# Kernel optimization log

Hardware: AMD Instinct MI355X
Metric: run time of the kernel (lower is better)

## Reference

```python
import jax, jax.numpy as jnp
import numpy as np

N_NODES = 50000
N_EDGES = 800000


def setup_inputs() -> dict:
    key = jax.random.key(0)
    k1, k2, k3, k4 = jax.random.split(key, 4)
    x = jax.random.normal(k1, (N_NODES, 100), dtype=jnp.float32)
    edge_index = jax.random.randint(k2, (2, N_EDGES), 0, N_NODES, dtype=jnp.int64)
    W1 = jax.random.normal(k3, (100, 128), dtype=jnp.float32) * 0.1
    b1 = jnp.zeros((128,), dtype=jnp.float32)
    W2 = jax.random.normal(k4, (128, 64), dtype=jnp.float32) * 0.1
    b2 = jnp.zeros((64,), dtype=jnp.float32)
    return {"x": x, "edge_index": edge_index, "W1": W1, "b1": b1, "W2": W2, "b2": b2}


def _gcn_norm(edge_index, n_nodes):
    # PyG GCNConv default: add self-loops, then symmetric normalization
    row, col = edge_index[0], edge_index[1]
    loop = jnp.arange(n_nodes, dtype=row.dtype)
    row = jnp.concatenate([row, loop])
    col = jnp.concatenate([col, loop])
    deg = jax.ops.segment_sum(jnp.ones_like(col, dtype=jnp.float32), col,
                              num_segments=n_nodes)
    dinv = jnp.where(deg > 0, jax.lax.rsqrt(deg), 0.0)
    norm = dinv[row] * dinv[col]  # [E + N]
    return row, col, norm


def _gcn_conv(x, W, b, row, col, norm, n_nodes):
    h = x @ W                       # [N, out] linear transform first (PyG order)
    msg = norm[:, None] * h[row]    # gather + scale over edges
    agg = jax.ops.segment_sum(msg, col, num_segments=n_nodes)  # scatter-add
    return agg + b


def reference(x, edge_index, W1, b1, W2, b2):
    n = x.shape[0]
    row, col, norm = _gcn_norm(edge_index, n)
    h = _gcn_conv(x, W1, b1, row, col, norm, n)
    h = jax.nn.relu(h)
    out = _gcn_conv(h, W2, b2, row, col, norm, n)
    return out
```

## Files before the change

kernel.cpp:

```cpp
#include <hip/hip_runtime.h>
#include <hip/hip_fp16.h>

#define DIV_UP(a,b) (((a)+(b)-1)/(b))

typedef _Float16 half8 __attribute__((ext_vector_type(8)));
typedef float f32x4 __attribute__((ext_vector_type(4)));

#define BUK_BITS 8
#define BUK_SIZE 256
#define BUK_CAP  6144
#define CSR_CAP  8192
#define MAXBUK   256
#define NBLK_BUCKET 256
#define CHUNK_MAX 3136

#define SWZ(row, colh) ((colh) ^ (((row) & 7) << 3))


__device__ __forceinline__ int edge_at(const void* ei, int mode64, int idx) {
  if (mode64) return (int)((const long long*)ei)[idx];
  return ((const int*)ei)[idx];
}

__global__ __launch_bounds__(256) void k_init(int* __restrict__ bcur,
                                              const float* __restrict__ W1,
                                              const float* __restrict__ W2,
                                              _Float16* __restrict__ Wt1,
                                              _Float16* __restrict__ Wt2) {
  int i = blockIdx.x * 256 + threadIdx.x;
  if (i < MAXBUK) bcur[i] = 0;
  if (i < 128 * 128) {
    int nc = i >> 7, k = i & 127;
    Wt1[i] = (k < 100) ? (_Float16)W1[k * 128 + nc] : (_Float16)0.f;
  } else if (i < 128 * 128 + 64 * 128) {
    int j = i - 128 * 128;
    int nc = j >> 7, k = j & 127;
    Wt2[j] = (_Float16)W2[k * 64 + nc];
  }
}

__global__ __launch_bounds__(256) void k_bucket(const void* __restrict__ ei,
                                                int* __restrict__ bcur,
                                                unsigned int* __restrict__ recs,
                                                int E, int nbuk) {
  __shared__ unsigned int lrec[CHUNK_MAX];
  __shared__ unsigned int sorted[CHUNK_MAX];
  __shared__ int hist[MAXBUK], lofs[MAXBUK], gbase[MAXBUK], cur[MAXBUK];
  __shared__ int smode;

  if (threadIdx.x < 64) {
    int v = ((const int*)ei)[2 * threadIdx.x + 1];
    unsigned long long b = __ballot(v == 0);
    if (threadIdx.x == 0) smode = (b == ~0ull) ? 1 : 0;
  }
  for (int i = threadIdx.x; i < nbuk; i += 256) hist[i] = 0;
  __syncthreads();
  const int m = smode;

  const int chunk = DIV_UP(E, gridDim.x);
  const int e0 = blockIdx.x * chunk;
  const int cnt = min(E, e0 + chunk) - e0;
  if (cnt <= 0) return;

  for (int i = threadIdx.x; i < cnt; i += 256) {
    int r = edge_at(ei, m, e0 + i);
    int c = edge_at(ei, m, E + e0 + i);
    unsigned int rec = ((unsigned)c << 16) | (unsigned)r;
    lrec[i] = rec;
    atomicAdd(&hist[c >> BUK_BITS], 1);
  }
  __syncthreads();

  if (threadIdx.x == 0) {
    int run = 0;
    for (int b = 0; b < nbuk; ++b) { lofs[b] = run; run += hist[b]; }
  }
  __syncthreads();
  for (int b = threadIdx.x; b < nbuk; b += 256) {
    gbase[b] = b * BUK_CAP + atomicAdd(&bcur[b], hist[b]);
    cur[b] = lofs[b];
  }
  __syncthreads();

  for (int i = threadIdx.x; i < cnt; i += 256) {
    unsigned int rec = lrec[i];
    int b = rec >> (16 + BUK_BITS);
    int p = atomicAdd(&cur[b], 1);
    sorted[p] = rec;
  }
  __syncthreads();

  for (int i = threadIdx.x; i < cnt; i += 256) {
    unsigned int rec = sorted[i];
    int b = rec >> (16 + BUK_BITS);
    recs[gbase[b] + i - lofs[b]] = rec;
  }
}

__global__ __launch_bounds__(256) void k_bdeg_fill(const int* __restrict__ bcur,
                                                   const unsigned int* __restrict__ recs,
                                                   float* __restrict__ dinv,
                                                   int2* __restrict__ rowinfo,
                                                   unsigned short* __restrict__ csr,
                                                   int n) {
  __shared__ int h[BUK_SIZE];
  __shared__ int psum[BUK_SIZE];
  __shared__ int curs[BUK_SIZE];
  __shared__ unsigned short lcsr[CSR_CAP];

  const int b = blockIdx.x, tid = threadIdx.x;
  const int base = b * BUK_CAP;
  const int cnt = bcur[b];
  const int n0 = b << BUK_BITS;
  const int nn = min(BUK_SIZE, n - n0);

  h[tid] = 0;
  __syncthreads();
  for (int i = tid; i < cnt; i += 256)
    atomicAdd(&h[(int)(recs[base + i] >> 16) - n0], 1);
  __syncthreads();

  const int deg = h[tid];
  const int plen = (deg + 7) & ~7;
  psum[tid] = plen;
  __syncthreads();
#pragma unroll
  for (int off2 = 1; off2 < 256; off2 <<= 1) {
    int v = (tid >= off2) ? psum[tid - off2] : 0;
    __syncthreads();
    psum[tid] += v;
    __syncthreads();
  }
  const int excl = psum[tid] - plen;
  const int ptot = psum[255];

  if (tid < nn) {
    rowinfo[n0 + tid] = make_int2(b * CSR_CAP + excl, plen);
    dinv[n0 + tid] = rsqrtf((float)deg + 1.0f);
    curs[tid] = excl;
  }
  for (int i = tid; i < ptot; i += 256) lcsr[i] = (unsigned short)n;
  __syncthreads();

  for (int i = tid; i < cnt; i += 256) {
    unsigned int rec = recs[base + i];
    int cl = (int)(rec >> 16) - n0;
    int p = atomicAdd(&curs[cl], 1);
    lcsr[p] = (unsigned short)(rec & 0xFFFFu);
  }
  __syncthreads();
  for (int i = tid; i < ptot; i += 256) csr[b * CSR_CAP + i] = lcsr[i];
}

__global__ __launch_bounds__(256) void k_convx(const float4* __restrict__ x4,
                                               const float* __restrict__ dinv,
                                               uint2* __restrict__ xh4,
                                               uint2* __restrict__ thh2,
                                               int n, int total) {
  int i = blockIdx.x * 256 + threadIdx.x;
  if (i < total) {
    int node = i >> 5;
    int lane = i & 31;
    uint2 val = make_uint2(0u, 0u);
    if (node < n && lane < 25) {
      float d = dinv[node];
      float4 v = x4[node * 25 + lane];
      union { uint2 u; __half2 hh[2]; } p;
      p.hh[0] = __halves2half2(__float2half_rn(d * v.x), __float2half_rn(d * v.y));
      p.hh[1] = __halves2half2(__float2half_rn(d * v.z), __float2half_rn(d * v.w));
      val = p.u;
    }
    xh4[i] = val;
  } else {
    int s = i - total;
    if (s < 16) thh2[(n << 4) + s] = make_uint2(0u, 0u);
  }
}

__device__ __forceinline__ float4 h4_to_f4(uint2 u) {
  union { uint2 u; __half2 h[2]; } p; p.u = u;
  float2 a = __half22float2(p.h[0]);
  float2 b = __half22float2(p.h[1]);
  return make_float4(a.x, a.y, b.x, b.y);
}
__device__ __forceinline__ void acc_add(float4& acc, float4 a) {
  acc.x += a.x; acc.y += a.y; acc.z += a.z; acc.w += a.w;
}

__global__ __launch_bounds__(256) void k_pull1(const int2* __restrict__ rowinfo,
                                               const unsigned short* __restrict__ csr,
                                               const uint2* __restrict__ xh4,
                                               const float* __restrict__ dinv,
                                               uint2* __restrict__ aggh4, int n) {
  int g = threadIdx.x / 25;
  int lane = threadIdx.x - g * 25;
  if (g >= 10) return;
  int node = blockIdx.x * 10 + g;
  if (node >= n) return;

  float4 acc = h4_to_f4(xh4[(node << 5) + lane]);
  int2 ri = rowinfo[node];
  int beg = ri.x, end = ri.x + ri.y;
  int j = beg;
  for (; j + 16 <= end; j += 16) {
    uint4 cw0 = *(const uint4*)&csr[j];
    uint4 cw1 = *(const uint4*)&csr[j + 8];
    int r0 = cw0.x & 0xFFFF, r1 = cw0.x >> 16;
    int r2 = cw0.y & 0xFFFF, r3 = cw0.y >> 16;
    int r4 = cw0.z & 0xFFFF, r5 = cw0.z >> 16;
    int r6 = cw0.w & 0xFFFF, r7 = cw0.w >> 16;
    int r8 = cw1.x & 0xFFFF, r9 = cw1.x >> 16;
    int rA = cw1.y & 0xFFFF, rB = cw1.y >> 16;
    int rC = cw1.z & 0xFFFF, rD = cw1.z >> 16;
    int rE = cw1.w & 0xFFFF, rF = cw1.w >> 16;
    float4 t0 = h4_to_f4(xh4[(r0 << 5) + lane]);
    float4 t1 = h4_to_f4(xh4[(r1 << 5) + lane]);
    float4 t2 = h4_to_f4(xh4[(r2 << 5) + lane]);
    float4 t3 = h4_to_f4(xh4[(r3 << 5) + lane]);
    float4 t4 = h4_to_f4(xh4[(r4 << 5) + lane]);
    float4 t5 = h4_to_f4(xh4[(r5 << 5) + lane]);
    float4 t6 = h4_to_f4(xh4[(r6 << 5) + lane]);
    float4 t7 = h4_to_f4(xh4[(r7 << 5) + lane]);
    float4 t8 = h4_to_f4(xh4[(r8 << 5) + lane]);
    float4 t9 = h4_to_f4(xh4[(r9 << 5) + lane]);
    float4 tA = h4_to_f4(xh4[(rA << 5) + lane]);
    float4 tB = h4_to_f4(xh4[(rB << 5) + lane]);
    float4 tC = h4_to_f4(xh4[(rC << 5) + lane]);
    float4 tD = h4_to_f4(xh4[(rD << 5) + lane]);
    float4 tE = h4_to_f4(xh4[(rE << 5) + lane]);
    float4 tF = h4_to_f4(xh4[(rF << 5) + lane]);
    acc_add(acc, t0); acc_add(acc, t1); acc_add(acc, t2); acc_add(acc, t3);
    acc_add(acc, t4); acc_add(acc, t5); acc_add(acc, t6); acc_add(acc, t7);
    acc_add(acc, t8); acc_add(acc, t9); acc_add(acc, tA); acc_add(acc, tB);
    acc_add(acc, tC); acc_add(acc, tD); acc_add(acc, tE); acc_add(acc, tF);
  }
  if (j < end) {
    uint4 cw = *(const uint4*)&csr[j];
    int r0 = cw.x & 0xFFFF, r1 = cw.x >> 16;
    int r2 = cw.y & 0xFFFF, r3 = cw.y >> 16;
    int r4 = cw.z & 0xFFFF, r5 = cw.z >> 16;
    int r6 = cw.w & 0xFFFF, r7 = cw.w >> 16;
    float4 t0 = h4_to_f4(xh4[(r0 << 5) + lane]);
    float4 t1 = h4_to_f4(xh4[(r1 << 5) + lane]);
    float4 t2 = h4_to_f4(xh4[(r2 << 5) + lane]);
    float4 t3 = h4_to_f4(xh4[(r3 << 5) + lane]);
    float4 t4 = h4_to_f4(xh4[(r4 << 5) + lane]);
    float4 t5 = h4_to_f4(xh4[(r5 << 5) + lane]);
    float4 t6 = h4_to_f4(xh4[(r6 << 5) + lane]);
    float4 t7 = h4_to_f4(xh4[(r7 << 5) + lane]);
    acc_add(acc, t0); acc_add(acc, t1); acc_add(acc, t2); acc_add(acc, t3);
    acc_add(acc, t4); acc_add(acc, t5); acc_add(acc, t6); acc_add(acc, t7);
  }
  float d = dinv[node];
  union { uint2 u; __half2 h[2]; } p;
  p.h[0] = __halves2half2(__float2half_rn(d * acc.x), __float2half_rn(d * acc.y));
  p.h[1] = __halves2half2(__float2half_rn(d * acc.z), __float2half_rn(d * acc.w));
  aggh4[(node << 5) + lane] = p.u;
  if (lane < 7) aggh4[(node << 5) + 25 + lane] = make_uint2(0u, 0u);
}

__global__ __launch_bounds__(256) void k_pull2(const int2* __restrict__ rowinfo,
                                               const unsigned short* __restrict__ csr,
                                               const uint4* __restrict__ th4,
                                               const float* __restrict__ dinv,
                                               const float4* __restrict__ b2_4,
                                               float4* __restrict__ out4, int n) {
  int g = threadIdx.x >> 3;
  int lane = threadIdx.x & 7;
  int node = blockIdx.x * 32 + g;
  if (node >= n) return;

  uint4 sv = th4[(node << 3) + lane];
  float4 acc0 = h4_to_f4(make_uint2(sv.x, sv.y));
  float4 acc1 = h4_to_f4(make_uint2(sv.z, sv.w));

  int2 ri = rowinfo[node];
  int beg = ri.x, end = ri.x + ri.y;
  int j = beg;
  for (; j + 16 <= end; j += 16) {
    uint4 cw0 = *(const uint4*)&csr[j];
    uint4 cw1 = *(const uint4*)&csr[j + 8];
    int r0 = cw0.x & 0xFFFF, r1 = cw0.x >> 16;
    int r2 = cw0.y & 0xFFFF, r3 = cw0.y >> 16;
    int r4 = cw0.z & 0xFFFF, r5 = cw0.z >> 16;
    int r6 = cw0.w & 0xFFFF, r7 = cw0.w >> 16;
    int r8 = cw1.x & 0xFFFF, r9 = cw1.x >> 16;
    int rA = cw1.y & 0xFFFF, rB = cw1.y >> 16;
    int rC = cw1.z & 0xFFFF, rD = cw1.z >> 16;
    int rE = cw1.w & 0xFFFF, rF = cw1.w >> 16;
    uint4 u0 = th4[(r0 << 3) + lane];
    uint4 u1 = th4[(r1 << 3) + lane];
    uint4 u2 = th4[(r2 << 3) + lane];
    uint4 u3 = th4[(r3 << 3) + lane];
    uint4 u4 = th4[(r4 << 3) + lane];
    uint4 u5 = th4[(r5 << 3) + lane];
    uint4 u6 = th4[(r6 << 3) + lane];
    uint4 u7 = th4[(r7 << 3) + lane];
    uint4 u8 = th4[(r8 << 3) + lane];
    uint4 u9 = th4[(r9 << 3) + lane];
    uint4 uA = th4[(rA << 3) + lane];
    uint4 uB = th4[(rB << 3) + lane];
    uint4 uC = th4[(rC << 3) + lane];
    uint4 uD = th4[(rD << 3) + lane];
    uint4 uE = th4[(rE << 3) + lane];
    uint4 uF = th4[(rF << 3) + lane];
    acc_add(acc0, h4_to_f4(make_uint2(u0.x, u0.y)));
    acc_add(acc1, h4_to_f4(make_uint2(u0.z, u0.w)));
    acc_add(acc0, h4_to_f4(make_uint2(u1.x, u1.y)));
    acc_add(acc1, h4_to_f4(make_uint2(u1.z, u1.w)));
    acc_add(acc0, h4_to_f4(make_uint2(u2.x, u2.y)));
    acc_add(acc1, h4_to_f4(make_uint2(u2.z, u2.w)));
    acc_add(acc0, h4_to_f4(make_uint2(u3.x, u3.y)));
    acc_add(acc1, h4_to_f4(make_uint2(u3.z, u3.w)));
    acc_add(acc0, h4_to_f4(make_uint2(u4.x, u4.y)));
    acc_add(acc1, h4_to_f4(make_uint2(u4.z, u4.w)));
    acc_add(acc0, h4_to_f4(make_uint2(u5.x, u5.y)));
    acc_add(acc1, h4_to_f4(make_uint2(u5.z, u5.w)));
    acc_add(acc0, h4_to_f4(make_uint2(u6.x, u6.y)));
    acc_add(acc1, h4_to_f4(make_uint2(u6.z, u6.w)));
    acc_add(acc0, h4_to_f4(make_uint2(u7.x, u7.y)));
    acc_add(acc1, h4_to_f4(make_uint2(u7.z, u7.w)));
    acc_add(acc0, h4_to_f4(make_uint2(u8.x, u8.y)));
    acc_add(acc1, h4_to_f4(make_uint2(u8.z, u8.w)));
    acc_add(acc0, h4_to_f4(make_uint2(u9.x, u9.y)));
    acc_add(acc1, h4_to_f4(make_uint2(u9.z, u9.w)));
    acc_add(acc0, h4_to_f4(make_uint2(uA.x, uA.y)));
    acc_add(acc1, h4_to_f4(make_uint2(uA.z, uA.w)));
    acc_add(acc0, h4_to_f4(make_uint2(uB.x, uB.y)));
    acc_add(acc1, h4_to_f4(make_uint2(uB.z, uB.w)));
    acc_add(acc0, h4_to_f4(make_uint2(uC.x, uC.y)));
    acc_add(acc1, h4_to_f4(make_uint2(uC.z, uC.w)));
    acc_add(acc0, h4_to_f4(make_uint2(uD.x, uD.y)));
    acc_add(acc1, h4_to_f4(make_uint2(uD.z, uD.w)));
    acc_add(acc0, h4_to_f4(make_uint2(uE.x, uE.y)));
    acc_add(acc1, h4_to_f4(make_uint2(uE.z, uE.w)));
    acc_add(acc0, h4_to_f4(make_uint2(uF.x, uF.y)));
    acc_add(acc1, h4_to_f4(make_uint2(uF.z, uF.w)));
  }
  if (j < end) {
    uint4 cw = *(const uint4*)&csr[j];
    int r0 = cw.x & 0xFFFF, r1 = cw.x >> 16;
    int r2 = cw.y & 0xFFFF, r3 = cw.y >> 16;
    int r4 = cw.z & 0xFFFF, r5 = cw.z >> 16;
    int r6 = cw.w & 0xFFFF, r7 = cw.w >> 16;
    uint4 u0 = th4[(r0 << 3) + lane];
    uint4 u1 = th4[(r1 << 3) + lane];
    uint4 u2 = th4[(r2 << 3) + lane];
    uint4 u3 = th4[(r3 << 3) + lane];
    uint4 u4 = th4[(r4 << 3) + lane];
    uint4 u5 = th4[(r5 << 3) + lane];
    uint4 u6 = th4[(r6 << 3) + lane];
    uint4 u7 = th4[(r7 << 3) + lane];
    acc_add(acc0, h4_to_f4(make_uint2(u0.x, u0.y)));
    acc_add(acc1, h4_to_f4(make_uint2(u0.z, u0.w)));
    acc_add(acc0, h4_to_f4(make_uint2(u1.x, u1.y)));
    acc_add(acc1, h4_to_f4(make_uint2(u1.z, u1.w)));
    acc_add(acc0, h4_to_f4(make_uint2(u2.x, u2.y)));
    acc_add(acc1, h4_to_f4(make_uint2(u2.z, u2.w)));
    acc_add(acc0, h4_to_f4(make_uint2(u3.x, u3.y)));
    acc_add(acc1, h4_to_f4(make_uint2(u3.z, u3.w)));
    acc_add(acc0, h4_to_f4(make_uint2(u4.x, u4.y)));
    acc_add(acc1, h4_to_f4(make_uint2(u4.z, u4.w)));
    acc_add(acc0, h4_to_f4(make_uint2(u5.x, u5.y)));
    acc_add(acc1, h4_to_f4(make_uint2(u5.z, u5.w)));
    acc_add(acc0, h4_to_f4(make_uint2(u6.x, u6.y)));
    acc_add(acc1, h4_to_f4(make_uint2(u6.z, u6.w)));
    acc_add(acc0, h4_to_f4(make_uint2(u7.x, u7.y)));
    acc_add(acc1, h4_to_f4(make_uint2(u7.z, u7.w)));
  }
  float d = dinv[node];
  float4 bb0 = b2_4[lane * 2], bb1 = b2_4[lane * 2 + 1];
  out4[(node << 4) + lane * 2]     = make_float4(d * acc0.x + bb0.x, d * acc0.y + bb0.y,
                                                 d * acc0.z + bb0.z, d * acc0.w + bb0.w);
  out4[(node << 4) + lane * 2 + 1] = make_float4(d * acc1.x + bb1.x, d * acc1.y + bb1.y,
                                                 d * acc1.z + bb1.z, d * acc1.w + bb1.w);
}

__global__ __launch_bounds__(256, 2) void k_gemmf(const _Float16* __restrict__ A,
                                                  const _Float16* __restrict__ Wt1,
                                                  const float* __restrict__ b1,
                                                  const _Float16* __restrict__ Wt2,
                                                  const float* __restrict__ dinv,
                                                  _Float16* __restrict__ thh, int n) {
  __shared__ __align__(16) _Float16 lds[4][16 * 128];
  const int wid = threadIdx.x >> 6;
  const int lane = threadIdx.x & 63;
  const int lr = lane & 15;
  const int lk = lane >> 4;
  _Float16* myl = lds[wid];

  half8 B1[8][4];
#pragma unroll
  for (int nt = 0; nt < 8; ++nt)
#pragma unroll
    for (int ks = 0; ks < 4; ++ks)
      B1[nt][ks] = *(const half8*)&Wt1[(nt * 16 + lr) * 128 + ks * 32 + lk * 8];
  float bs[8];
#pragma unroll
  for (int nt = 0; nt < 8; ++nt) bs[nt] = b1[nt * 16 + lr];

  const int nstrips = (n + 15) >> 4;
  for (int s = blockIdx.x * 4 + wid; s < nstrips; s += gridDim.x * 4) {
    const int arow = s * 16 + lr;
    half8 a[4];
#pragma unroll
    for (int ks = 0; ks < 4; ++ks)
      a[ks] = (arow < n) ? *(const half8*)&A[(size_t)arow * 128 + ks * 32 + lk * 8]
                         : half8{0, 0, 0, 0, 0, 0, 0, 0};
    f32x4 acc[8];
#pragma unroll
    for (int nt = 0; nt < 8; ++nt) acc[nt] = f32x4{0.f, 0.f, 0.f, 0.f};
#pragma unroll
    for (int ks = 0; ks < 4; ++ks)
#pragma unroll
      for (int nt = 0; nt < 8; ++nt)
        acc[nt] = __builtin_amdgcn_mfma_f32_16x16x32_f16(a[ks], B1[nt][ks], acc[nt], 0, 0, 0);

#pragma unroll
    for (int r = 0; r < 4; ++r) {
      int row = lk * 4 + r;
#pragma unroll
      for (int nt = 0; nt < 8; ++nt)
        myl[row * 128 + SWZ(row, nt * 16 + lr)] =
            (_Float16)fmaxf(acc[nt][r] + bs[nt], 0.f);
    }

    half8 B2[4][4];
#pragma unroll
    for (int nt = 0; nt < 4; ++nt)
#pragma unroll
      for (int ks = 0; ks < 4; ++ks)
        B2[nt][ks] = *(const half8*)&Wt2[(nt * 16 + lr) * 128 + ks * 32 + lk * 8];

    half8 a2[4];
#pragma unroll
    for (int ks = 0; ks < 4; ++ks)
      a2[ks] = *(const half8*)&myl[lr * 128 + SWZ(lr, ks * 32 + lk * 8)];

    f32x4 acc2[4];
#pragma unroll
    for (int nt = 0; nt < 4; ++nt) acc2[nt] = f32x4{0.f, 0.f, 0.f, 0.f};
#pragma unroll
    for (int ks = 0; ks < 4; ++ks)
#pragma unroll
      for (int nt = 0; nt < 4; ++nt)
        acc2[nt] = __builtin_amdgcn_mfma_f32_16x16x32_f16(a2[ks], B2[nt][ks], acc2[nt], 0, 0, 0);

    const int rb = s * 16 + lk * 4;
    float sc[4];
    if (rb + 3 < n) {
      const float4 dv = *(const float4*)&dinv[rb];
      sc[0] = dv.x; sc[1] = dv.y; sc[2] = dv.z; sc[3] = dv.w;
    } else {
#pragma unroll
      for (int r = 0; r < 4; ++r) sc[r] = (rb + r < n) ? dinv[rb + r] : 0.f;
    }
#pragma unroll
    for (int r = 0; r < 4; ++r) {
      const int orow = rb + r;
      if (orow < n) {
#pragma unroll
        for (int nt = 0; nt < 4; ++nt)
          thh[(size_t)orow * 64 + nt * 16 + lr] = (_Float16)(acc2[nt][r] * sc[r]);
      }
    }
  }
}

extern "C" void kernel_launch(void* const* d_in, const int* in_sizes, int n_in,
                              void* d_out, int out_size, void* d_ws, size_t ws_size,
                              hipStream_t stream) {
  const float* x  = (const float*)d_in[0];
  const void*  ei = d_in[1];
  const float* W1 = (const float*)d_in[2];
  const float* b1 = (const float*)d_in[3];
  const float* W2 = (const float*)d_in[4];
  const float* b2 = (const float*)d_in[5];
  float* out = (float*)d_out;

  const int n = in_sizes[0] / 100;
  const int E = in_sizes[1] / 2;
  const int nbuk = DIV_UP(n, BUK_SIZE);

  char* ws = (char*)d_ws;
  size_t off = 0;
  auto alloc = [&](size_t bytes) { void* p = ws + off; off += (bytes + 15) & ~15ull; return p; };
  int*            bcur     = (int*)   alloc(MAXBUK * 4);
  float*          dinv     = (float*) alloc((size_t)n * 4);
  int2*           rowinfo  = (int2*)  alloc((size_t)n * 8);
  unsigned int*   recs     = (unsigned int*)alloc((size_t)nbuk * BUK_CAP * 4);
  unsigned short* csr      = (unsigned short*)alloc((size_t)nbuk * CSR_CAP * 2);
  _Float16*       xh       = (_Float16*)alloc((size_t)(n + 1) * 128 * 2);
  _Float16*       aggh     = (_Float16*)alloc((size_t)n * 128 * 2);
  _Float16*       thh      = (_Float16*)alloc((size_t)(n + 1) * 64 * 2);
  _Float16*       Wt1h     = (_Float16*)alloc(128 * 128 * 2);
  _Float16*       Wt2h     = (_Float16*)alloc(64 * 128 * 2);

  k_init<<<97, 256, 0, stream>>>(bcur, W1, W2, Wt1h, Wt2h);
  k_bucket<<<NBLK_BUCKET, 256, 0, stream>>>(ei, bcur, recs, E, nbuk);
  k_bdeg_fill<<<nbuk, 256, 0, stream>>>(bcur, recs, dinv, rowinfo, csr, n);

  const int total = (n + 1) * 32;
  k_convx<<<DIV_UP(total + 16, 256), 256, 0, stream>>>((const float4*)x, dinv,
      (uint2*)xh, (uint2*)thh, n, total);

  k_pull1<<<DIV_UP(n, 10), 256, 0, stream>>>(rowinfo, csr, (const uint2*)xh, dinv,
                                             (uint2*)aggh, n);
  const int nstrips = DIV_UP(n, 16);
  k_gemmf<<<DIV_UP(nstrips, 8), 256, 0, stream>>>(aggh, Wt1h, b1, Wt2h, dinv, thh, n);
  k_pull2<<<DIV_UP(n, 32), 256, 0, stream>>>(rowinfo, csr, (const uint4*)thh, dinv,
                                             (const float4*)b2, (float4*)out, n);
}
```

Measured before the change: 118.7 us.

## Split first-layer gather into two feature-half passes for cache locality

The first aggregation kernel is split into two launches, each gathering 16 of the 32 uint2 feature chunks per node with 16 lanes per node. The gathered working set per pass is halved so it is more likely to stay resident in L2/MALL during the random neighbor gathers. In exchange, the CSR indices and rowinfo are read twice and there is an extra launch. Padding chunks 25..31 are now computed from the zero-padded input rather than written as explicit zeros, which adds some wasted gather work.

```diff
diff --git a/kernel.cpp b/kernel.cpp
--- a/kernel.cpp
+++ b/kernel.cpp
@@ -187,18 +187,19 @@
   acc.x += a.x; acc.y += a.y; acc.z += a.z; acc.w += a.w;
 }
 
-__global__ __launch_bounds__(256) void k_pull1(const int2* __restrict__ rowinfo,
-                                               const unsigned short* __restrict__ csr,
-                                               const uint2* __restrict__ xh4,
-                                               const float* __restrict__ dinv,
-                                               uint2* __restrict__ aggh4, int n) {
-  int g = threadIdx.x / 25;
-  int lane = threadIdx.x - g * 25;
-  if (g >= 10) return;
-  int node = blockIdx.x * 10 + g;
+__global__ __launch_bounds__(256) void k_pull1h(const int2* __restrict__ rowinfo,
+                                                const unsigned short* __restrict__ csr,
+                                                const uint2* __restrict__ xh4,
+                                                const float* __restrict__ dinv,
+                                                uint2* __restrict__ aggh4,
+                                                int n, int sbase) {
+  int g = threadIdx.x >> 4;
+  int lane = threadIdx.x & 15;
+  int node = blockIdx.x * 16 + g;
   if (node >= n) return;
-
-  float4 acc = h4_to_f4(xh4[(node << 5) + lane]);
+  const int o = sbase + lane;
+
+  float4 acc = h4_to_f4(xh4[(node << 5) + o]);
   int2 ri = rowinfo[node];
   int beg = ri.x, end = ri.x + ri.y;
   int j = beg;
@@ -213,22 +214,22 @@
     int rA = cw1.y & 0xFFFF, rB = cw1.y >> 16;
     int rC = cw1.z & 0xFFFF, rD = cw1.z >> 16;
     int rE = cw1.w & 0xFFFF, rF = cw1.w >> 16;
-    float4 t0 = h4_to_f4(xh4[(r0 << 5) + lane]);
-    float4 t1 = h4_to_f4(xh4[(r1 << 5) + lane]);
-    float4 t2 = h4_to_f4(xh4[(r2 << 5) + lane]);
-    float4 t3 = h4_to_f4(xh4[(r3 << 5) + lane]);
-    float4 t4 = h4_to_f4(xh4[(r4 << 5) + lane]);
-    float4 t5 = h4_to_f4(xh4[(r5 << 5) + lane]);
-    float4 t6 = h4_to_f4(xh4[(r6 << 5) + lane]);
-    float4 t7 = h4_to_f4(xh4[(r7 << 5) + lane]);
-    float4 t8 = h4_to_f4(xh4[(r8 << 5) + lane]);
-    float4 t9 = h4_to_f4(xh4[(r9 << 5) + lane]);
-    float4 tA = h4_to_f4(xh4[(rA << 5) + lane]);
-    float4 tB = h4_to_f4(xh4[(rB << 5) + lane]);
-    float4 tC = h4_to_f4(xh4[(rC << 5) + lane]);
-    float4 tD = h4_to_f4(xh4[(rD << 5) + lane]);
-    float4 tE = h4_to_f4(xh4[(rE << 5) + lane]);
-    float4 tF = h4_to_f4(xh4[(rF << 5) + lane]);
+    float4 t0 = h4_to_f4(xh4[(r0 << 5) + o]);
+    float4 t1 = h4_to_f4(xh4[(r1 << 5) + o]);
+    float4 t2 = h4_to_f4(xh4[(r2 << 5) + o]);
+    float4 t3 = h4_to_f4(xh4[(r3 << 5) + o]);
+    float4 t4 = h4_to_f4(xh4[(r4 << 5) + o]);
+    float4 t5 = h4_to_f4(xh4[(r5 << 5) + o]);
+    float4 t6 = h4_to_f4(xh4[(r6 << 5) + o]);
+    float4 t7 = h4_to_f4(xh4[(r7 << 5) + o]);
+    float4 t8 = h4_to_f4(xh4[(r8 << 5) + o]);
+    float4 t9 = h4_to_f4(xh4[(r9 << 5) + o]);
+    float4 tA = h4_to_f4(xh4[(rA << 5) + o]);
+    float4 tB = h4_to_f4(xh4[(rB << 5) + o]);
+    float4 tC = h4_to_f4(xh4[(rC << 5) + o]);
+    float4 tD = h4_to_f4(xh4[(rD << 5) + o]);
+    float4 tE = h4_to_f4(xh4[(rE << 5) + o]);
+    float4 tF = h4_to_f4(xh4[(rF << 5) + o]);
     acc_add(acc, t0); acc_add(acc, t1); acc_add(acc, t2); acc_add(acc, t3);
     acc_add(acc, t4); acc_add(acc, t5); acc_add(acc, t6); acc_add(acc, t7);
     acc_add(acc, t8); acc_add(acc, t9); acc_add(acc, tA); acc_add(acc, tB);
@@ -240,14 +241,14 @@
     int r2 = cw.y & 0xFFFF, r3 = cw.y >> 16;
     int r4 = cw.z & 0xFFFF, r5 = cw.z >> 16;
     int r6 = cw.w & 0xFFFF, r7 = cw.w >> 16;
-    float4 t0 = h4_to_f4(xh4[(r0 << 5) + lane]);
-    float4 t1 = h4_to_f4(xh4[(r1 << 5) + lane]);
-    float4 t2 = h4_to_f4(xh4[(r2 << 5) + lane]);
-    float4 t3 = h4_to_f4(xh4[(r3 << 5) + lane]);
-    float4 t4 = h4_to_f4(xh4[(r4 << 5) + lane]);
-    float4 t5 = h4_to_f4(xh4[(r5 << 5) + lane]);
-    float4 t6 = h4_to_f4(xh4[(r6 << 5) + lane]);
-    float4 t7 = h4_to_f4(xh4[(r7 << 5) + lane]);
+    float4 t0 = h4_to_f4(xh4[(r0 << 5) + o]);
+    float4 t1 = h4_to_f4(xh4[(r1 << 5) + o]);
+    float4 t2 = h4_to_f4(xh4[(r2 << 5) + o]);
+    float4 t3 = h4_to_f4(xh4[(r3 << 5) + o]);
+    float4 t4 = h4_to_f4(xh4[(r4 << 5) + o]);
+    float4 t5 = h4_to_f4(xh4[(r5 << 5) + o]);
+    float4 t6 = h4_to_f4(xh4[(r6 << 5) + o]);
+    float4 t7 = h4_to_f4(xh4[(r7 << 5) + o]);
     acc_add(acc, t0); acc_add(acc, t1); acc_add(acc, t2); acc_add(acc, t3);
     acc_add(acc, t4); acc_add(acc, t5); acc_add(acc, t6); acc_add(acc, t7);
   }
@@ -255,8 +256,7 @@
   union { uint2 u; __half2 h[2]; } p;
   p.h[0] = __halves2half2(__float2half_rn(d * acc.x), __float2half_rn(d * acc.y));
   p.h[1] = __halves2half2(__float2half_rn(d * acc.z), __float2half_rn(d * acc.w));
-  aggh4[(node << 5) + lane] = p.u;
-  if (lane < 7) aggh4[(node << 5) + 25 + lane] = make_uint2(0u, 0u);
+  aggh4[(node << 5) + o] = p.u;
 }
 
 __global__ __launch_bounds__(256) void k_pull2(const int2* __restrict__ rowinfo,
@@ -504,8 +504,12 @@
   k_convx<<<DIV_UP(total + 16, 256), 256, 0, stream>>>((const float4*)x, dinv,
       (uint2*)xh, (uint2*)thh, n, total);
 
-  k_pull1<<<DIV_UP(n, 10), 256, 0, stream>>>(rowinfo, csr, (const uint2*)xh, dinv,
-                                             (uint2*)aggh, n);
+  const int nb1 = DIV_UP(n, 16);
+  k_pull1h<<<nb1, 256, 0, stream>>>(rowinfo, csr, (const uint2*)xh, dinv,
+                                    (uint2*)aggh, n, 0);
+  k_pull1h<<<nb1, 256, 0, stream>>>(rowinfo, csr, (const uint2*)xh, dinv,
+                                    (uint2*)aggh, n, 16);
+
   const int nstrips = DIV_UP(n, 16);
   k_gemmf<<<DIV_UP(nstrips, 8), 256, 0, stream>>>(aggh, Wt1h, b1, Wt2h, dinv, thh, n);
   k_pull2<<<DIV_UP(n, 32), 256, 0, stream>>>(rowinfo, csr, (const uint4*)thh, dinv,
```

New measurement: 133.9 us. +12.8%, slower.
